# Kernel tuning notes

Hardware: AMD Instinct MI355X
Metric: run time of the kernel (lower is better)

Reference implementation:

```python
import jax, jax.numpy as jnp
import numpy as np

WINDOW = 2048
STEP = WINDOW // 2                 # 1024
N_SAMPLES = 131072
N_COEFFS = WINDOW // 2 + 1         # 1025
N_FRAMES = N_SAMPLES // STEP       # 128
Z_DIM = 128
BATCH, N_EVENTS, IMP_SAMPLES = 64, 1, 4096
BASE_RES = 0.02
RES_RANGE = (1.0 - BASE_RES) * 0.99


def setup_inputs() -> dict:
    key = jax.random.key(0)
    k1, k2, k3 = jax.random.split(key, 3)
    z = jax.random.normal(k1, (BATCH, N_EVENTS, Z_DIM), dtype=jnp.float32)
    impulse = jax.random.normal(k2, (BATCH, N_EVENTS, IMP_SAMPLES), dtype=jnp.float32)
    # stand-in for ConvUpsample: linear z -> (n_coeffs * n_frames)
    W_tf = jax.random.normal(k3, (Z_DIM, N_COEFFS * N_FRAMES), dtype=jnp.float32) * 0.02
    b_tf = jnp.zeros((N_COEFFS * N_FRAMES,), dtype=jnp.float32)
    return {"z": z, "impulse": impulse, "W_tf": W_tf, "b_tf": b_tf}


def _hann(n):
    # periodic hann (torch.hann_window default)
    return (0.5 - 0.5 * jnp.cos(2.0 * jnp.pi * jnp.arange(n) / n)).astype(jnp.float32)


def reference(z, impulse, W_tf, b_tf):
    B, E, imp_len = impulse.shape
    pad = N_SAMPLES - imp_len + WINDOW
    x = jnp.pad(impulse, ((0, 0), (0, 0), (0, pad)))  # (B,E,n_samples+window)
    win = _hann(WINDOW)

    # windowed_audio: overlapping frames * hann window -> (B,E,F,W)
    idx = jnp.arange(N_FRAMES)[:, None] * STEP + jnp.arange(WINDOW)[None, :]
    windowed = x[..., idx] * win

    # transfer functions: linear, reshape (C,F) -> transpose to (F,C), squash
    tf = (z.reshape(-1, Z_DIM) @ W_tf + b_tf).reshape(B, E, N_COEFFS, N_FRAMES)
    tf = jnp.transpose(tf, (0, 1, 3, 2))                       # (B,E,F,C)
    tf = BASE_RES + jax.nn.sigmoid(tf) * RES_RANGE

    cur_specs = jnp.fft.rfft(windowed, axis=-1)                # (B,E,F,C) complex64

    # advance_one_frame rotation: [re,im] @ [[c,-s],[s,-c]]
    g = jnp.linspace(0.0, np.pi, N_COEFFS).astype(jnp.float32)
    c, s = jnp.cos(g), jnp.sin(g)

    def step(prev_audio, inp):
        cur_spec, tfi = inp
        ps = jnp.fft.rfft(prev_audio, axis=-1)
        re, im = ps.real, ps.imag
        rot = jax.lax.complex(re * c + im * s, -(re * s + im * c))
        spec = (cur_spec + rot) * tfi
        audio = jnp.fft.irfft(spec, n=WINDOW, axis=-1)
        return audio, audio

    xs = (jnp.moveaxis(cur_specs, 2, 0), jnp.moveaxis(tf, 2, 0))
    init = jnp.zeros((B, E, WINDOW), dtype=jnp.float32)  # i==0: zero prev spec
    _, frames = jax.lax.scan(step, init, xs)             # (F,B,E,W)
    frames = jnp.moveaxis(frames, 0, 2) * win            # overlap_add apply_window=True

    # overlap-add with hop = WINDOW//2, vectorized via half-frame reshapes
    first = frames[..., :STEP].reshape(B, E, N_FRAMES * STEP)
    second = frames[..., STEP:].reshape(B, E, N_FRAMES * STEP)
    out = jnp.zeros((B, E, (N_FRAMES + 1) * STEP), dtype=jnp.float32)
    out = out.at[..., : N_FRAMES * STEP].add(first)
    out = out.at[..., STEP:].add(second)
    return out[..., :N_SAMPLES]
```

## Files before the change

### kernel.cpp

```cpp
#include <hip/hip_runtime.h>

#define NB 64
#define ZDIM 128
#define NCOEF 1025
#define NFR 128
#define COLS 131200
#define WINSZ 2048
#define HALFW 1024
#define NSAMP 131072
#define IMPN 4096
#define NCHUNK 32
#define NCK 31

#define TF_OFF   0
#define TF_SZ    (NB*COLS)
#define TFT_OFF  (TF_OFF + TF_SZ)
#define TFT_SZ   (NB*NFR*NCOEF)
#define CUR_OFF  (TFT_OFF + TFT_SZ)
#define CUR_SZ   (NB*4*NCOEF*2)
#define CK_OFF   (CUR_OFF + CUR_SZ)
#define CK_SZ    (NCK*NB*NCOEF*2)
#define WINT_OFF (CK_OFF + CK_SZ)
#define WINT_SZ  (WINSZ)
#define TW_OFF   (WINT_OFF + WINT_SZ)
#define TW_SZ    (HALFW*2)

#define PHI(p) ((p) ^ ((((p) >> 4) & 3) << 2))

typedef short bf16x8 __attribute__((ext_vector_type(8)));
typedef float f32x4 __attribute__((ext_vector_type(4)));

__device__ __forceinline__ float2 cmul(float2 a, float2 b) {
  return make_float2(a.x * b.x - a.y * b.y, a.x * b.y + a.y * b.x);
}

__global__ __launch_bounds__(256) void init_tables(float* __restrict__ winT,
                                                   float2* __restrict__ twG) {
  int i = blockIdx.x * 256 + threadIdx.x;
  if (i < WINSZ) {
    winT[i] = 0.5f - 0.5f * cosf((float)(2.0 * 3.14159265358979323846 / 2048.0) * (float)i);
  }
  if (i < HALFW) {
    float ang = (float)(-2.0 * 3.14159265358979323846 / 2048.0) * (float)i;
    float sv, cv;
    sincosf(ang, &sv, &cv);
    twG[i] = make_float2(cv, sv);
  }
}

__device__ __forceinline__ short f2bf(float f) {
  unsigned u = __builtin_bit_cast(unsigned, f);
  u += 0x7FFFu + ((u >> 16) & 1u);
  return (short)(u >> 16);
}

__global__ __launch_bounds__(256) void tf_gemm_mfma(const float* __restrict__ z,
                                                    const float* __restrict__ W,
                                                    const float* __restrict__ bias,
                                                    float* __restrict__ tf) {
  int tid = threadIdx.x;
  int wave = tid >> 6, lane = tid & 63;
  int colw = blockIdx.x * 128 + wave * 32;
  int lr = lane & 15;
  int lk = (lane >> 4) * 8;
  int lq = (lane >> 4) * 4;

  float bv[2];
#pragma unroll
  for (int n = 0; n < 2; ++n) bv[n] = bias[colw + 16 * n + lr];

  f32x4 acc[4][2];
#pragma unroll
  for (int m = 0; m < 4; ++m)
#pragma unroll
    for (int n = 0; n < 2; ++n)
      acc[m][n] = f32x4{bv[n], bv[n], bv[n], bv[n]};

#pragma unroll
  for (int s = 0; s < 4; ++s) {
    int k0 = s * 32 + lk;
    bf16x8 afr[4];
#pragma unroll
    for (int m = 0; m < 4; ++m) {
      const float* zp = z + (size_t)(16 * m + lr) * ZDIM + k0;
      float4 z0 = *reinterpret_cast<const float4*>(zp);
      float4 z1 = *reinterpret_cast<const float4*>(zp + 4);
      afr[m] = bf16x8{f2bf(z0.x), f2bf(z0.y), f2bf(z0.z), f2bf(z0.w),
                      f2bf(z1.x), f2bf(z1.y), f2bf(z1.z), f2bf(z1.w)};
    }
    bf16x8 bfr[2];
#pragma unroll
    for (int n = 0; n < 2; ++n) {
      const float* wp = W + (size_t)k0 * COLS + colw + 16 * n + lr;
      bfr[n] = bf16x8{f2bf(wp[0 * (size_t)COLS]), f2bf(wp[1 * (size_t)COLS]),
                      f2bf(wp[2 * (size_t)COLS]), f2bf(wp[3 * (size_t)COLS]),
                      f2bf(wp[4 * (size_t)COLS]), f2bf(wp[5 * (size_t)COLS]),
                      f2bf(wp[6 * (size_t)COLS]), f2bf(wp[7 * (size_t)COLS])};
    }
#pragma unroll
    for (int m = 0; m < 4; ++m)
#pragma unroll
      for (int n = 0; n < 2; ++n)
        acc[m][n] = __builtin_amdgcn_mfma_f32_16x16x32_bf16(afr[m], bfr[n], acc[m][n], 0, 0, 0);
  }

  const float RESR = (1.0f - 0.02f) * 0.99f;
#pragma unroll
  for (int n = 0; n < 2; ++n) {
    int col = colw + 16 * n + lr;
#pragma unroll
    for (int m = 0; m < 4; ++m) {
      int rowb = 16 * m + lq;
#pragma unroll
      for (int r = 0; r < 4; ++r) {
        float x = acc[m][n][r];
        float sg = 1.0f / (1.0f + __expf(-x));
        tf[(size_t)(rowb + r) * COLS + col] = 0.02f + sg * RESR;
      }
    }
  }
}

static __device__ __forceinline__ void wg_fft2048(float* ar, float* ai,
                                                  float* br, float* bi,
                                                  const float2* tw,
                                                  float** outr, float** outi) {
  float *xr = ar, *xi = ai, *yr = br, *yi = bi;
  int m = 1;
  for (int s = 0; s < 11; ++s) {
    __syncthreads();
#pragma unroll
    for (int it = 0; it < 4; ++it) {
      int t = (int)threadIdx.x + it * 256;
      int jm = t & ~(m - 1);
      float x0r = xr[t], x0i = xi[t];
      float x1r = xr[t + 1024], x1i = xi[t + 1024];
      float2 w = tw[jm];
      float sr = x0r + x1r, si = x0i + x1i;
      float dr = x0r - x1r, di = x0i - x1i;
      float pr = dr * w.x - di * w.y;
      float pi = dr * w.y + di * w.x;
      yr[t + jm] = sr;      yi[t + jm] = si;
      yr[t + jm + m] = pr;  yi[t + jm + m] = pi;
    }
    float* t0 = xr; xr = yr; yr = t0;
    float* t1 = xi; xi = yi; yi = t1;
    m <<= 1;
  }
  __syncthreads();
  *outr = xr; *outi = xi;
}

__global__ __launch_bounds__(256) void fwd_fft_kernel(const float* __restrict__ imp,
                                                      const float* __restrict__ winT,
                                                      const float2* __restrict__ twG,
                                                      float2* __restrict__ cur) {
  __shared__ float b0r[WINSZ], b0i[WINSZ], b1r[WINSZ], b1i[WINSZ];
  __shared__ float2 tw[HALFW];
  int wg = blockIdx.x;
  int b = wg >> 2, f = wg & 3;
  int tid = threadIdx.x;

  for (int i = tid; i < HALFW; i += 256) tw[i] = twG[i];
  for (int w = tid; w < WINSZ; w += 256) {
    int s = f * HALFW + w;
    float v = (s < IMPN) ? imp[(size_t)b * IMPN + s] * winT[w] : 0.0f;
    b0r[w] = v;
    b0i[w] = 0.0f;
  }
  float *rr, *ri;
  wg_fft2048(b0r, b0i, b1r, b1i, tw, &rr, &ri);
  for (int k = tid; k < NCOEF; k += 256)
    cur[(size_t)wg * NCOEF + k] = make_float2(rr[k], ri[k]);
}

__global__ __launch_bounds__(256) void recur_ck_t(const float* __restrict__ tf,
                                                  const float2* __restrict__ cur,
                                                  float2* __restrict__ ckp,
                                                  float* __restrict__ tft) {
  int id = blockIdx.x * 256 + threadIdx.x;
  if (id >= NB * NCOEF) return;
  int b = id / NCOEF;
  int k = id - b * NCOEF;

  float g = 3.14159265358979323846f * (float)k / 1024.0f;
  float sg, cg;
  sincosf(g, &sg, &cg);
  bool herm = (k == 0) || (k == HALFW);

  const float4* tf4 = (const float4*)(tf + (size_t)b * COLS + (size_t)k * NFR);
  const float2* curb = cur + (size_t)b * 4 * NCOEF + k;
  float* tftb = tft + (size_t)b * NFR * NCOEF + k;

  float pre = 0.0f, pim = 0.0f;
  for (int f4 = 0; f4 < 32; ++f4) {
    float4 tv = tf4[f4];
    float tfs[4] = {tv.x, tv.y, tv.z, tv.w};
#pragma unroll
    for (int u = 0; u < 4; ++u) {
      int f = 4 * f4 + u;
      tftb[(size_t)f * NCOEF] = tfs[u];
      if (f < 124) {
        float tfv = tfs[u];
        float cr = 0.0f, ci = 0.0f;
        if (f < 4) {
          float2 cv = curb[(size_t)f * NCOEF];
          cr = cv.x; ci = cv.y;
        }
        float ire = herm ? 0.0f : pim;
        float rre = fmaf(pre, cg, ire * sg);
        float rim = -fmaf(pre, sg, ire * cg);
        float sre = (cr + rre) * tfv;
        float sim = (ci + rim) * tfv;
        if ((f & 3) == 2)
          ckp[(size_t)((f - 2) >> 2) * NB * NCOEF + (size_t)b * NCOEF + k] = make_float2(sre, sim);
        pre = sre; pim = sim;
      }
    }
  }
}

__global__ __launch_bounds__(256) void fused_resyn(const float* __restrict__ tft,
                                                   const float2* __restrict__ cur,
                                                   const float2* __restrict__ ckp,
                                                   const float* __restrict__ winT,
                                                   const float2* __restrict__ twG,
                                                   float* __restrict__ out) {
  __shared__ float2 P[1024];

  int bidx = blockIdx.x;
  int b = bidx >> 5, c = bidx & 31;
  int t = threadIdx.x;

  float pre[5], pim[5], cgv[5], sgv[5];
#pragma unroll
  for (int i = 0; i < 5; ++i) {
    if (i == 4) { cgv[4] = -1.0f; sgv[4] = 0.0f; }
    else {
      float2 tv = twG[t + 256 * i];
      cgv[i] = tv.x; sgv[i] = -tv.y;
    }
    pre[i] = 0.0f; pim[i] = 0.0f;
  }
  if (c > 0) {
    const float2* ck = ckp + ((size_t)(c - 1) * NB + b) * NCOEF;
#pragma unroll
    for (int i = 0; i < 5; ++i) {
      if (i == 4 && t != 0) continue;
      int k = (i == 4) ? 1024 : t + 256 * i;
      float2 v = ck[k];
      pre[i] = v.x; pim[i] = v.y;
    }
  }

  float2 w1a = twG[2 * t];            float2 w1b = cmul(w1a, w1a); float2 w1c = cmul(w1b, w1a);
  float2 w2a = twG[8 * (t & 63)];     float2 w2b = cmul(w2a, w2a); float2 w2c = cmul(w2b, w2a);
  float2 w3a = twG[32 * (t & 15)];    float2 w3b = cmul(w3a, w3a); float2 w3c = cmul(w3b, w3a);
  float2 w4a = twG[128 * (t & 3)];    float2 w4b = cmul(w4a, w4a); float2 w4c = cmul(w4b, w4a);
  float2 twp0 = twG[t], twp1 = twG[t + 256], twp2 = twG[t + 512], twp3 = twG[t + 768];

  int mb = (t >> 6) + ((t >> 4) & 3) * 4 + ((t >> 2) & 3) * 16 + (t & 3) * 64;
  const float2* win2 = (const float2*)winT;
  float2 wv0 = win2[mb], wv1 = win2[mb + 256], wv2 = win2[mb + 512], wv3 = win2[mb + 768];

  int X0 = PHI(t);
  int B2 = 256 * (t >> 6) + ((t & 63) ^ (((t >> 4) & 3) << 2));
  int b3h = 64 * (t >> 4), i3 = t & 15;
  int b4h = 16 * (t >> 2), i4 = t & 3, c4 = (t >> 2) & 3;
  int p5 = b4h + 4 * ((t & 3) ^ c4);
  int pm0 = PHI((1024 - t) & 1023);
  int pm1 = PHI((1024 - (t + 256)) & 1023);
  int pm2 = PHI((1024 - (t + 512)) & 1023);
  int pm3 = PHI((1024 - (t + 768)) & 1023);

  const float* tftb = tft + (size_t)b * NFR * NCOEF;
  const float2* curb = cur + (size_t)b * 4 * NCOEF;
  const float Cs = 0.5f / 1024.0f;

  int fs = (c == 0) ? 0 : 4 * c - 1;
  int fe = 4 * c + 3;
  float carE0 = 0.0f, carO0 = 0.0f, carE1 = 0.0f, carO1 = 0.0f;

  for (int f = fs; f <= fe; ++f) {
    float S[5], I[5];
    {
      const float* tfr = tftb + (size_t)f * NCOEF;
#pragma unroll
      for (int i = 0; i < 5; ++i) {
        if (i == 4 && t != 0) { S[4] = 0.0f; I[4] = 0.0f; continue; }
        int k = (i == 4) ? 1024 : t + 256 * i;
        float tfv = tfr[k];
        float cr = 0.0f, ci = 0.0f;
        if (f < 4) {
          float2 cv = curb[(size_t)f * NCOEF + k];
          cr = cv.x; ci = cv.y;
        }
        float rre = fmaf(pre[i], cgv[i], pim[i] * sgv[i]);
        float rim = -fmaf(pre[i], sgv[i], pim[i] * cgv[i]);
        S[i] = (cr + rre) * tfv;
        I[i] = (ci + rim) * tfv;
        pre[i] = S[i]; pim[i] = I[i];
      }
    }

    __syncthreads();
#pragma unroll
    for (int i = 0; i < 4; ++i)
      P[X0 + 256 * i] = make_float2(S[i], I[i]);
    __syncthreads();

    float2 Z[4];
    {
      float2 xm[4];
      xm[0] = (t == 0) ? make_float2(S[4], 0.0f) : P[pm0];
      xm[1] = P[pm1]; xm[2] = P[pm2]; xm[3] = P[pm3];
      float2 twp[4] = {twp0, twp1, twp2, twp3};
#pragma unroll
      for (int i = 0; i < 4; ++i) {
        float xjr = S[i], xji = I[i];
        float cc = twp[i].x, sn = -twp[i].y;
        float Xer = Cs * (xjr + xm[i].x), Xei = Cs * (xji - xm[i].y);
        float Xpr = Cs * (xjr - xm[i].x), Xpi = Cs * (xji + xm[i].y);
        float Xor_ = Xpr * cc - Xpi * sn;
        float Xoi_ = Xpr * sn + Xpi * cc;
        Z[i] = make_float2(Xer - Xoi_, -(Xei + Xor_));
      }
    }
    float2 y0, y1, y2, y3;
    {
      float2 A = make_float2(Z[0].x + Z[2].x, Z[0].y + Z[2].y);
      float2 Bv = make_float2(Z[0].x - Z[2].x, Z[0].y - Z[2].y);
      float2 Cv = make_float2(Z[1].x + Z[3].x, Z[1].y + Z[3].y);
      float2 D = make_float2(Z[1].x - Z[3].x, Z[1].y - Z[3].y);
      y0 = make_float2(A.x + Cv.x, A.y + Cv.y);
      y1 = cmul(make_float2(Bv.x + D.y, Bv.y - D.x), w1a);
      y2 = cmul(make_float2(A.x - Cv.x, A.y - Cv.y), w1b);
      y3 = cmul(make_float2(Bv.x - D.y, Bv.y + D.x), w1c);
    }
    __syncthreads();
    P[X0]       = y0;
    P[X0 + 256] = y1;
    P[X0 + 512] = y2;
    P[X0 + 768] = y3;
    __syncthreads();

    float2 u0 = P[B2], u1 = P[B2 + 64], u2 = P[B2 + 128], u3 = P[B2 + 192];
    {
      float2 A = make_float2(u0.x + u2.x, u0.y + u2.y);
      float2 Bv = make_float2(u0.x - u2.x, u0.y - u2.y);
      float2 Cv = make_float2(u1.x + u3.x, u1.y + u3.y);
      float2 D = make_float2(u1.x - u3.x, u1.y - u3.y);
      P[B2]       = make_float2(A.x + Cv.x, A.y + Cv.y);
      P[B2 + 64]  = cmul(make_float2(Bv.x + D.y, Bv.y - D.x), w2a);
      P[B2 + 128] = cmul(make_float2(A.x - Cv.x, A.y - Cv.y), w2b);
      P[B2 + 192] = cmul(make_float2(Bv.x - D.y, Bv.y + D.x), w2c);
    }
    asm volatile("s_waitcnt lgkmcnt(0)" ::: "memory");

    u0 = P[b3h + i3];
    u1 = P[b3h + 16 + (i3 ^ 4)];
    u2 = P[b3h + 32 + (i3 ^ 8)];
    u3 = P[b3h + 48 + (i3 ^ 12)];
    {
      float2 A = make_float2(u0.x + u2.x, u0.y + u2.y);
      float2 Bv = make_float2(u0.x - u2.x, u0.y - u2.y);
      float2 Cv = make_float2(u1.x + u3.x, u1.y + u3.y);
      float2 D = make_float2(u1.x - u3.x, u1.y - u3.y);
      P[b3h + i3]             = make_float2(A.x + Cv.x, A.y + Cv.y);
      P[b3h + 16 + (i3 ^ 4)]  = cmul(make_float2(Bv.x + D.y, Bv.y - D.x), w3a);
      P[b3h + 32 + (i3 ^ 8)]  = cmul(make_float2(A.x - Cv.x, A.y - Cv.y), w3b);
      P[b3h + 48 + (i3 ^ 12)] = cmul(make_float2(Bv.x - D.y, Bv.y + D.x), w3c);
    }
    asm volatile("s_waitcnt lgkmcnt(0)" ::: "memory");

    u0 = P[b4h + 4 * (0 ^ c4) + i4];
    u1 = P[b4h + 4 * (1 ^ c4) + i4];
    u2 = P[b4h + 4 * (2 ^ c4) + i4];
    u3 = P[b4h + 4 * (3 ^ c4) + i4];
    {
      float2 A = make_float2(u0.x + u2.x, u0.y + u2.y);
      float2 Bv = make_float2(u0.x - u2.x, u0.y - u2.y);
      float2 Cv = make_float2(u1.x + u3.x, u1.y + u3.y);
      float2 D = make_float2(u1.x - u3.x, u1.y - u3.y);
      P[b4h + 4 * (0 ^ c4) + i4] = make_float2(A.x + Cv.x, A.y + Cv.y);
      P[b4h + 4 * (1 ^ c4) + i4] = cmul(make_float2(Bv.x + D.y, Bv.y - D.x), w4a);
      P[b4h + 4 * (2 ^ c4) + i4] = cmul(make_float2(A.x - Cv.x, A.y - Cv.y), w4b);
      P[b4h + 4 * (3 ^ c4) + i4] = cmul(make_float2(Bv.x - D.y, Bv.y + D.x), w4c);
    }
    asm volatile("s_waitcnt lgkmcnt(0)" ::: "memory");

    float4 q01 = *reinterpret_cast<const float4*>(&P[p5]);
    float4 q23 = *reinterpret_cast<const float4*>(&P[p5 + 2]);
    float2 z0, z1, z2, z3;
    {
      float2 a = make_float2(q01.x, q01.y), bq = make_float2(q01.z, q01.w);
      float2 cq = make_float2(q23.x, q23.y), d = make_float2(q23.z, q23.w);
      float2 A = make_float2(a.x + cq.x, a.y + cq.y);
      float2 Bv = make_float2(a.x - cq.x, a.y - cq.y);
      float2 Cv = make_float2(bq.x + d.x, bq.y + d.y);
      float2 D = make_float2(bq.x - d.x, bq.y - d.y);
      z0 = make_float2(A.x + Cv.x, A.y + Cv.y);
      z1 = make_float2(Bv.x + D.y, Bv.y - D.x);
      z2 = make_float2(A.x - Cv.x, A.y - Cv.y);
      z3 = make_float2(Bv.x - D.y, Bv.y + D.x);
    }

    float e0 = z0.x * wv0.x, o0 = -z0.y * wv0.y;
    float e1 = z1.x * wv1.x, o1 = -z1.y * wv1.y;
    float e2 = z2.x * wv2.x, o2 = -z2.y * wv2.y;
    float e3 = z3.x * wv3.x, o3 = -z3.y * wv3.y;
    if (f >= 4 * c) {
      float2* ob2 = (float2*)(out + (size_t)b * NSAMP + (size_t)f * 1024);
      ob2[mb]       = make_float2(e0 + carE0, o0 + carO0);
      ob2[mb + 256] = make_float2(e1 + carE1, o1 + carO1);
    }
    carE0 = e2; carO0 = o2;
    carE1 = e3; carO1 = o3;
  }
}

extern "C" void kernel_launch(void* const* d_in, const int* in_sizes, int n_in,
                              void* d_out, int out_size, void* d_ws, size_t ws_size,
                              hipStream_t stream) {
  const float* z    = (const float*)d_in[0];
  const float* imp  = (const float*)d_in[1];
  const float* W    = (const float*)d_in[2];
  const float* bias = (const float*)d_in[3];

  float* ws = (float*)d_ws;
  float*  tf   = ws + TF_OFF;
  float*  tft  = ws + TFT_OFF;
  float2* cur  = (float2*)(ws + CUR_OFF);
  float2* ckp  = (float2*)(ws + CK_OFF);
  float*  winT = ws + WINT_OFF;
  float2* twG  = (float2*)(ws + TW_OFF);
  float*  out  = (float*)d_out;

  init_tables<<<8, 256, 0, stream>>>(winT, twG);
  tf_gemm_mfma<<<COLS / 128, 256, 0, stream>>>(z, W, bias, tf);
  fwd_fft_kernel<<<NB * 4, 256, 0, stream>>>(imp, winT, twG, cur);
  recur_ck_t<<<(NB * NCOEF + 255) / 256, 256, 0, stream>>>(tf, cur, ckp, tft);
  fused_resyn<<<NB * NCHUNK, 256, 0, stream>>>(tft, cur, ckp, winT, twG, out);
}
```

Baseline: 96.27 us.

## Prefetch GEMM and resynthesis loads, pre-convert z to bf16, double-buffer LDS

The GEMM kernel now issues all W loads up front and reads z from a bf16 copy produced once in init_tables, so the per-wave float-to-bf16 conversion of z is no longer repeated and more loads are in flight. The resynthesis kernel software-prefetches the next frame's transfer-function and spectrum values into registers, and moves FFT stages 2 onward into a second LDS buffer, which removes one barrier per frame. Lightweight barrier macros and occupancy hints are added. The cost is higher register pressure and more shared memory per block, which could lower occupancy.

```diff
diff --git a/kernel.cpp b/kernel.cpp
--- a/kernel.cpp
+++ b/kernel.cpp
@@ -24,6 +24,8 @@
 #define WINT_SZ  (WINSZ)
 #define TW_OFF   (WINT_OFF + WINT_SZ)
 #define TW_SZ    (HALFW*2)
+#define ZBF_OFF  (TW_OFF + TW_SZ)
+#define ZBF_SZ   (NB*ZDIM/2)
 
 #define PHI(p) ((p) ^ ((((p) >> 4) & 3) << 2))
 
@@ -34,8 +36,23 @@
   return make_float2(a.x * b.x - a.y * b.y, a.x * b.y + a.y * b.x);
 }
 
-__global__ __launch_bounds__(256) void init_tables(float* __restrict__ winT,
-                                                   float2* __restrict__ twG) {
+#define WGBAR()                                              \
+  do {                                                       \
+    asm volatile("s_waitcnt lgkmcnt(0)" ::: "memory");       \
+    __builtin_amdgcn_s_barrier();                            \
+    asm volatile("" ::: "memory");                           \
+  } while (0)
+
+__device__ __forceinline__ short f2bf(float f) {
+  unsigned u = __builtin_bit_cast(unsigned, f);
+  u += 0x7FFFu + ((u >> 16) & 1u);
+  return (short)(u >> 16);
+}
+
+__global__ __launch_bounds__(256) void init_tables(const float* __restrict__ z,
+                                                   float* __restrict__ winT,
+                                                   float2* __restrict__ twG,
+                                                   short* __restrict__ zbf) {
   int i = blockIdx.x * 256 + threadIdx.x;
   if (i < WINSZ) {
     winT[i] = 0.5f - 0.5f * cosf((float)(2.0 * 3.14159265358979323846 / 2048.0) * (float)i);
@@ -46,18 +63,13 @@
     sincosf(ang, &sv, &cv);
     twG[i] = make_float2(cv, sv);
   }
-}
-
-__device__ __forceinline__ short f2bf(float f) {
-  unsigned u = __builtin_bit_cast(unsigned, f);
-  u += 0x7FFFu + ((u >> 16) & 1u);
-  return (short)(u >> 16);
-}
-
-__global__ __launch_bounds__(256) void tf_gemm_mfma(const float* __restrict__ z,
-                                                    const float* __restrict__ W,
-                                                    const float* __restrict__ bias,
-                                                    float* __restrict__ tf) {
+  if (i < NB * ZDIM) zbf[i] = f2bf(z[i]);
+}
+
+__global__ __launch_bounds__(256, 2) void tf_gemm_mfma(const short* __restrict__ zbf,
+                                                       const float* __restrict__ W,
+                                                       const float* __restrict__ bias,
+                                                       float* __restrict__ tf) {
   int tid = threadIdx.x;
   int wave = tid >> 6, lane = tid & 63;
   int colw = blockIdx.x * 128 + wave * 32;
@@ -65,6 +77,24 @@
   int lk = (lane >> 4) * 8;
   int lq = (lane >> 4) * 4;
 
+  float wf[4][2][8];
+#pragma unroll
+  for (int s = 0; s < 4; ++s)
+#pragma unroll
+    for (int n = 0; n < 2; ++n) {
+      const float* wp = W + (size_t)(s * 32 + lk) * COLS + colw + 16 * n + lr;
+#pragma unroll
+      for (int j = 0; j < 8; ++j)
+        wf[s][n][j] = wp[(size_t)j * COLS];
+    }
+
+  bf16x8 afr[4][4];
+#pragma unroll
+  for (int s = 0; s < 4; ++s)
+#pragma unroll
+    for (int m = 0; m < 4; ++m)
+      afr[s][m] = *reinterpret_cast<const bf16x8*>(zbf + (16 * m + lr) * ZDIM + s * 32 + lk);
+
   float bv[2];
 #pragma unroll
   for (int n = 0; n < 2; ++n) bv[n] = bias[colw + 16 * n + lr];
@@ -78,30 +108,16 @@
 
 #pragma unroll
   for (int s = 0; s < 4; ++s) {
-    int k0 = s * 32 + lk;
-    bf16x8 afr[4];
-#pragma unroll
-    for (int m = 0; m < 4; ++m) {
-      const float* zp = z + (size_t)(16 * m + lr) * ZDIM + k0;
-      float4 z0 = *reinterpret_cast<const float4*>(zp);
-      float4 z1 = *reinterpret_cast<const float4*>(zp + 4);
-      afr[m] = bf16x8{f2bf(z0.x), f2bf(z0.y), f2bf(z0.z), f2bf(z0.w),
-                      f2bf(z1.x), f2bf(z1.y), f2bf(z1.z), f2bf(z1.w)};
-    }
     bf16x8 bfr[2];
 #pragma unroll
-    for (int n = 0; n < 2; ++n) {
-      const float* wp = W + (size_t)k0 * COLS + colw + 16 * n + lr;
-      bfr[n] = bf16x8{f2bf(wp[0 * (size_t)COLS]), f2bf(wp[1 * (size_t)COLS]),
-                      f2bf(wp[2 * (size_t)COLS]), f2bf(wp[3 * (size_t)COLS]),
-                      f2bf(wp[4 * (size_t)COLS]), f2bf(wp[5 * (size_t)COLS]),
-                      f2bf(wp[6 * (size_t)COLS]), f2bf(wp[7 * (size_t)COLS])};
-    }
+    for (int n = 0; n < 2; ++n)
+      bfr[n] = bf16x8{f2bf(wf[s][n][0]), f2bf(wf[s][n][1]), f2bf(wf[s][n][2]), f2bf(wf[s][n][3]),
+                      f2bf(wf[s][n][4]), f2bf(wf[s][n][5]), f2bf(wf[s][n][6]), f2bf(wf[s][n][7])};
 #pragma unroll
     for (int m = 0; m < 4; ++m)
 #pragma unroll
       for (int n = 0; n < 2; ++n)
-        acc[m][n] = __builtin_amdgcn_mfma_f32_16x16x32_bf16(afr[m], bfr[n], acc[m][n], 0, 0, 0);
+        acc[m][n] = __builtin_amdgcn_mfma_f32_16x16x32_bf16(afr[s][m], bfr[n], acc[m][n], 0, 0, 0);
   }
 
   const float RESR = (1.0f - 0.02f) * 0.99f;
@@ -220,13 +236,14 @@
   }
 }
 
-__global__ __launch_bounds__(256) void fused_resyn(const float* __restrict__ tft,
-                                                   const float2* __restrict__ cur,
-                                                   const float2* __restrict__ ckp,
-                                                   const float* __restrict__ winT,
-                                                   const float2* __restrict__ twG,
-                                                   float* __restrict__ out) {
+__global__ __launch_bounds__(256, 6) void fused_resyn(const float* __restrict__ tft,
+                                                      const float2* __restrict__ cur,
+                                                      const float2* __restrict__ ckp,
+                                                      const float* __restrict__ winT,
+                                                      const float2* __restrict__ twG,
+                                                      float* __restrict__ out) {
   __shared__ float2 P[1024];
+  __shared__ float2 Q[1024];
 
   int bidx = blockIdx.x;
   int b = bidx >> 5, c = bidx & 31;
@@ -281,33 +298,68 @@
   int fe = 4 * c + 3;
   float carE0 = 0.0f, carO0 = 0.0f, carE1 = 0.0f, carO1 = 0.0f;
 
+  float ntf[5];
+  float2 ncur[4];
+  float2 ncur4;
+  {
+    const float* tfr = tftb + (size_t)fs * NCOEF;
+#pragma unroll
+    for (int i = 0; i < 4; ++i) ntf[i] = tfr[t + 256 * i];
+    ntf[4] = (t == 0) ? tfr[1024] : 0.0f;
+    if (fs < 4) {
+#pragma unroll
+      for (int i = 0; i < 4; ++i) ncur[i] = curb[(size_t)fs * NCOEF + t + 256 * i];
+      ncur4 = (t == 0) ? curb[(size_t)fs * NCOEF + 1024] : make_float2(0.0f, 0.0f);
+    } else {
+#pragma unroll
+      for (int i = 0; i < 4; ++i) ncur[i] = make_float2(0.0f, 0.0f);
+      ncur4 = make_float2(0.0f, 0.0f);
+    }
+  }
+
   for (int f = fs; f <= fe; ++f) {
+    float ctf[5];
+    float2 ccur[4];
+    float2 ccur4 = ncur4;
+#pragma unroll
+    for (int i = 0; i < 5; ++i) ctf[i] = ntf[i];
+#pragma unroll
+    for (int i = 0; i < 4; ++i) ccur[i] = ncur[i];
+
+    if (f < fe) {
+      int fn = f + 1;
+      const float* tfr = tftb + (size_t)fn * NCOEF;
+#pragma unroll
+      for (int i = 0; i < 4; ++i) ntf[i] = tfr[t + 256 * i];
+      ntf[4] = (t == 0) ? tfr[1024] : 0.0f;
+      if (fn < 4) {
+#pragma unroll
+        for (int i = 0; i < 4; ++i) ncur[i] = curb[(size_t)fn * NCOEF + t + 256 * i];
+        ncur4 = (t == 0) ? curb[(size_t)fn * NCOEF + 1024] : make_float2(0.0f, 0.0f);
+      } else {
+#pragma unroll
+        for (int i = 0; i < 4; ++i) ncur[i] = make_float2(0.0f, 0.0f);
+        ncur4 = make_float2(0.0f, 0.0f);
+      }
+    }
+
     float S[5], I[5];
-    {
-      const float* tfr = tftb + (size_t)f * NCOEF;
-#pragma unroll
-      for (int i = 0; i < 5; ++i) {
-        if (i == 4 && t != 0) { S[4] = 0.0f; I[4] = 0.0f; continue; }
-        int k = (i == 4) ? 1024 : t + 256 * i;
-        float tfv = tfr[k];
-        float cr = 0.0f, ci = 0.0f;
-        if (f < 4) {
-          float2 cv = curb[(size_t)f * NCOEF + k];
-          cr = cv.x; ci = cv.y;
-        }
-        float rre = fmaf(pre[i], cgv[i], pim[i] * sgv[i]);
-        float rim = -fmaf(pre[i], sgv[i], pim[i] * cgv[i]);
-        S[i] = (cr + rre) * tfv;
-        I[i] = (ci + rim) * tfv;
-        pre[i] = S[i]; pim[i] = I[i];
-      }
-    }
-
-    __syncthreads();
+#pragma unroll
+    for (int i = 0; i < 5; ++i) {
+      if (i == 4 && t != 0) { S[4] = 0.0f; I[4] = 0.0f; continue; }
+      float cr = (i == 4) ? ccur4.x : ccur[i].x;
+      float ci = (i == 4) ? ccur4.y : ccur[i].y;
+      float rre = fmaf(pre[i], cgv[i], pim[i] * sgv[i]);
+      float rim = -fmaf(pre[i], sgv[i], pim[i] * cgv[i]);
+      S[i] = (cr + rre) * ctf[i];
+      I[i] = (ci + rim) * ctf[i];
+      pre[i] = S[i]; pim[i] = I[i];
+    }
+
 #pragma unroll
     for (int i = 0; i < 4; ++i)
       P[X0 + 256 * i] = make_float2(S[i], I[i]);
-    __syncthreads();
+    WGBAR();
 
     float2 Z[4];
     {
@@ -337,60 +389,61 @@
       y2 = cmul(make_float2(A.x - Cv.x, A.y - Cv.y), w1b);
       y3 = cmul(make_float2(Bv.x - D.y, Bv.y + D.x), w1c);
     }
-    __syncthreads();
-    P[X0]       = y0;
-    P[X0 + 256] = y1;
-    P[X0 + 512] = y2;
-    P[X0 + 768] = y3;
-    __syncthreads();
-
-    float2 u0 = P[B2], u1 = P[B2 + 64], u2 = P[B2 + 128], u3 = P[B2 + 192];
+    WGBAR();
+    P[X0];
+    Q[X0]       = y0;
+    Q[X0 + 256] = y1;
+    Q[X0 + 512] = y2;
+    Q[X0 + 768] = y3;
+    WGBAR();
+
+    float2 u0 = Q[B2], u1 = Q[B2 + 64], u2 = Q[B2 + 128], u3 = Q[B2 + 192];
     {
       float2 A = make_float2(u0.x + u2.x, u0.y + u2.y);
       float2 Bv = make_float2(u0.x - u2.x, u0.y - u2.y);
       float2 Cv = make_float2(u1.x + u3.x, u1.y + u3.y);
       float2 D = make_float2(u1.x - u3.x, u1.y - u3.y);
-      P[B2]       = make_float2(A.x + Cv.x, A.y + Cv.y);
-      P[B2 + 64]  = cmul(make_float2(Bv.x + D.y, Bv.y - D.x), w2a);
-      P[B2 + 128] = cmul(make_float2(A.x - Cv.x, A.y - Cv.y), w2b);
-      P[B2 + 192] = cmul(make_float2(Bv.x - D.y, Bv.y + D.x), w2c);
+      Q[B2]       = make_float2(A.x + Cv.x, A.y + Cv.y);
+      Q[B2 + 64]  = cmul(make_float2(Bv.x + D.y, Bv.y - D.x), w2a);
+      Q[B2 + 128] = cmul(make_float2(A.x - Cv.x, A.y - Cv.y), w2b);
+      Q[B2 + 192] = cmul(make_float2(Bv.x - D.y, Bv.y + D.x), w2c);
     }
     asm volatile("s_waitcnt lgkmcnt(0)" ::: "memory");
 
-    u0 = P[b3h + i3];
-    u1 = P[b3h + 16 + (i3 ^ 4)];
-    u2 = P[b3h + 32 + (i3 ^ 8)];
-    u3 = P[b3h + 48 + (i3 ^ 12)];
+    u0 = Q[b3h + i3];
+    u1 = Q[b3h + 16 + (i3 ^ 4)];
+    u2 = Q[b3h + 32 + (i3 ^ 8)];
+    u3 = Q[b3h + 48 + (i3 ^ 12)];
     {
       float2 A = make_float2(u0.x + u2.x, u0.y + u2.y);
       float2 Bv = make_float2(u0.x - u2.x, u0.y - u2.y);
       float2 Cv = make_float2(u1.x + u3.x, u1.y + u3.y);
       float2 D = make_float2(u1.x - u3.x, u1.y - u3.y);
-      P[b3h + i3]             = make_float2(A.x + Cv.x, A.y + Cv.y);
-      P[b3h + 16 + (i3 ^ 4)]  = cmul(make_float2(Bv.x + D.y, Bv.y - D.x), w3a);
-      P[b3h + 32 + (i3 ^ 8)]  = cmul(make_float2(A.x - Cv.x, A.y - Cv.y), w3b);
-      P[b3h + 48 + (i3 ^ 12)] = cmul(make_float2(Bv.x - D.y, Bv.y + D.x), w3c);
+      Q[b3h + i3]             = make_float2(A.x + Cv.x, A.y + Cv.y);
+      Q[b3h + 16 + (i3 ^ 4)]  = cmul(make_float2(Bv.x + D.y, Bv.y - D.x), w3a);
+      Q[b3h + 32 + (i3 ^ 8)]  = cmul(make_float2(A.x - Cv.x, A.y - Cv.y), w3b);
+      Q[b3h + 48 + (i3 ^ 12)] = cmul(make_float2(Bv.x - D.y, Bv.y + D.x), w3c);
     }
     asm volatile("s_waitcnt lgkmcnt(0)" ::: "memory");
 
-    u0 = P[b4h + 4 * (0 ^ c4) + i4];
-    u1 = P[b4h + 4 * (1 ^ c4) + i4];
-    u2 = P[b4h + 4 * (2 ^ c4) + i4];
-    u3 = P[b4h + 4 * (3 ^ c4) + i4];
+    u0 = Q[b4h + 4 * (0 ^ c4) + i4];
+    u1 = Q[b4h + 4 * (1 ^ c4) + i4];
+    u2 = Q[b4h + 4 * (2 ^ c4) + i4];
+    u3 = Q[b4h + 4 * (3 ^ c4) + i4];
     {
       float2 A = make_float2(u0.x + u2.x, u0.y + u2.y);
       float2 Bv = make_float2(u0.x - u2.x, u0.y - u2.y);
       float2 Cv = make_float2(u1.x + u3.x, u1.y + u3.y);
       float2 D = make_float2(u1.x - u3.x, u1.y - u3.y);
-      P[b4h + 4 * (0 ^ c4) + i4] = make_float2(A.x + Cv.x, A.y + Cv.y);
-      P[b4h + 4 * (1 ^ c4) + i4] = cmul(make_float2(Bv.x + D.y, Bv.y - D.x), w4a);
-      P[b4h + 4 * (2 ^ c4) + i4] = cmul(make_float2(A.x - Cv.x, A.y - Cv.y), w4b);
-      P[b4h + 4 * (3 ^ c4) + i4] = cmul(make_float2(Bv.x - D.y, Bv.y + D.x), w4c);
+      Q[b4h + 4 * (0 ^ c4) + i4] = make_float2(A.x + Cv.x, A.y + Cv.y);
+      Q[b4h + 4 * (1 ^ c4) + i4] = cmul(make_float2(Bv.x + D.y, Bv.y - D.x), w4a);
+      Q[b4h + 4 * (2 ^ c4) + i4] = cmul(make_float2(A.x - Cv.x, A.y - Cv.y), w4b);
+      Q[b4h + 4 * (3 ^ c4) + i4] = cmul(make_float2(Bv.x - D.y, Bv.y + D.x), w4c);
     }
     asm volatile("s_waitcnt lgkmcnt(0)" ::: "memory");
 
-    float4 q01 = *reinterpret_cast<const float4*>(&P[p5]);
-    float4 q23 = *reinterpret_cast<const float4*>(&P[p5 + 2]);
+    float4 q01 = *reinterpret_cast<const float4*>(&Q[p5]);
+    float4 q23 = *reinterpret_cast<const float4*>(&Q[p5 + 2]);
     float2 z0, z1, z2, z3;
     {
       float2 a = make_float2(q01.x, q01.y), bq = make_float2(q01.z, q01.w);
@@ -434,10 +487,11 @@
   float2* ckp  = (float2*)(ws + CK_OFF);
   float*  winT = ws + WINT_OFF;
   float2* twG  = (float2*)(ws + TW_OFF);
+  short*  zbf  = (short*)(ws + ZBF_OFF);
   float*  out  = (float*)d_out;
 
-  init_tables<<<8, 256, 0, stream>>>(winT, twG);
-  tf_gemm_mfma<<<COLS / 128, 256, 0, stream>>>(z, W, bias, tf);
+  init_tables<<<32, 256, 0, stream>>>(z, winT, twG, zbf);
+  tf_gemm_mfma<<<COLS / 128, 256, 0, stream>>>(zbf, W, bias, tf);
   fwd_fft_kernel<<<NB * 4, 256, 0, stream>>>(imp, winT, twG, cur);
   recur_ck_t<<<(NB * NCOEF + 255) / 256, 256, 0, stream>>>(tf, cur, ckp, tft);
   fused_resyn<<<NB * NCHUNK, 256, 0, stream>>>(tft, cur, ckp, winT, twG, out);
```

After: 188.3 us. +95.6%, slower.
